# Optimization experiments

Measured on AMD Instinct MI355X. Metric: run time of the kernel, lower is better.

Reference implementation:

```python
import jax, jax.numpy as jnp
import numpy as np

TEMPERATURE = 0.1


def setup_inputs() -> dict:
    key = jax.random.key(0)
    k1, k2 = jax.random.split(key)
    N, T, D = 4096, 4, 256
    v_feat = jax.random.normal(k1, (N, D), dtype=jnp.float32)
    t_feat = jax.random.normal(k2, (N * T, D), dtype=jnp.float32)
    return {"v_feat": v_feat, "t_feat": t_feat}


def reference(v_feat, t_feat):
    N, D = v_feat.shape
    NT = t_feat.shape[0]
    T = NT // N

    # similarity matrix, scaled by temperature: [N, N*T]
    s_flat = (v_feat @ t_feat.T) / TEMPERATURE
    s = s_flat.reshape(N, N, T)

    # nominator: diagonal blocks s[i, i, :] -> logsumexp over T
    # (equivalent to (s * eye[:, :, None]).sum(dim=1))
    diag = jnp.diagonal(s, axis1=0, axis2=1).T  # [N, T]
    nominator = jax.nn.logsumexp(diag, axis=1)  # [N]

    # denominator: concat(s, s^T) along dim 1 -> [N, 2N, T] -> logsumexp over flat
    denom_in = jnp.concatenate([s, jnp.transpose(s, (1, 0, 2))], axis=1).reshape(N, -1)
    denominator = jax.nn.logsumexp(denom_in, axis=1)  # [N]

    mil_nce_loss = jnp.mean(denominator - nominator)

    # --- metrics (no grad), vectorized replacement of the python loop ---
    # rank[i, j] = index (into N*T columns) of the j-th largest score for row i
    rank = jnp.argsort(-s_flat, axis=1)  # [N, N*T], descending
    # column c belongs to video c // T; positive hit where that equals row index i
    hit = (rank // T) == jnp.arange(N)[:, None]  # [N, N*T] bool
    positions = jnp.arange(NT, dtype=jnp.float32)
    avg_rank = jnp.sum(hit.astype(jnp.float32) * positions, axis=1) / T
    recall1 = jnp.sum(hit[:, :1].astype(jnp.float32), axis=1) / T
    recall5 = jnp.sum(hit[:, :5].astype(jnp.float32), axis=1) / T
    recall10 = jnp.sum(hit[:, :10].astype(jnp.float32), axis=1) / T

    return (mil_nce_loss,
            jnp.mean(recall1), jnp.mean(recall5), jnp.mean(recall10),
            jnp.mean(avg_rank))
```

## Files before the change

### kernel.cpp

```cpp
#include <hip/hip_runtime.h>
#include <stdint.h>

#define N_V   4096
#define T_PER 4
#define NT    16384
#define D_K   256
#define SCALE 10.0f
#define LOG2E 1.44269504088896340736f
#define LN2   0.69314718055994530942f

#if defined(__has_builtin)
#if __has_builtin(__builtin_amdgcn_exp2f)
#define EXP2F(x) __builtin_amdgcn_exp2f(x)
#endif
#endif
#ifndef EXP2F
#define EXP2F(x) exp2f(x)
#endif

typedef __bf16 bf16x8 __attribute__((ext_vector_type(8)));
typedef float  f32x4  __attribute__((ext_vector_type(4)));

template<int C>
__device__ __forceinline__ float dppf(float v) {
  return __int_as_float(__builtin_amdgcn_update_dpp(
      0, __float_as_int(v), C, 0xf, 0xf, true));
}
template<int C>
__device__ __forceinline__ uint32_t dppu(uint32_t v) {
  return (uint32_t)__builtin_amdgcn_update_dpp(0, (int)v, C, 0xf, 0xf, true);
}
__device__ __forceinline__ float max16(float v) {
  v = fmaxf(v, dppf<0x121>(v));
  v = fmaxf(v, dppf<0x122>(v));
  v = fmaxf(v, dppf<0x124>(v));
  v = fmaxf(v, dppf<0x128>(v));
  return v;
}
__device__ __forceinline__ float sum16f(float v) {
  v += dppf<0x121>(v); v += dppf<0x122>(v);
  v += dppf<0x124>(v); v += dppf<0x128>(v);
  return v;
}
__device__ __forceinline__ uint32_t sum16u(uint32_t v) {
  v += dppu<0x121>(v); v += dppu<0x122>(v);
  v += dppu<0x124>(v); v += dppu<0x128>(v);
  return v;
}

__device__ __forceinline__ unsigned short f2bf(float f) {
  uint32_t u = __float_as_uint(f);
  u = (u + 0x7fffu + ((u >> 16) & 1u)) >> 16;
  return (unsigned short)u;
}

__global__ void k_prep(const float* __restrict__ v, const float* __restrict__ t,
                       unsigned short* __restrict__ Abf, unsigned short* __restrict__ Bbf,
                       float* __restrict__ thr, float* __restrict__ nom,
                       float* __restrict__ out) {
  const int tid = threadIdx.x, l = tid & 63, w = tid >> 6;
  const int i = blockIdx.x * 4 + w;
  if (blockIdx.x == 0 && tid < 5) out[tid] = 0.0f;
  const float AS = SCALE * LOG2E;

  float4 a = ((const float4*)(v + (size_t)i * D_K))[l];
  ushort4 oa;
  oa.x = f2bf(a.x * AS); oa.y = f2bf(a.y * AS);
  oa.z = f2bf(a.z * AS); oa.w = f2bf(a.w * AS);
  ((ushort4*)(Abf + (size_t)i * D_K))[l] = oa;

  float tv[T_PER];
#pragma unroll
  for (int tt = 0; tt < T_PER; ++tt) {
    float4 b = ((const float4*)(t + (size_t)(i * T_PER + tt) * D_K))[l];
    ushort4 ob;
    ob.x = f2bf(b.x); ob.y = f2bf(b.y); ob.z = f2bf(b.z); ob.w = f2bf(b.w);
    ((ushort4*)(Bbf + (size_t)(i * T_PER + tt) * D_K))[l] = ob;
    float d = a.x * b.x + a.y * b.y + a.z * b.z + a.w * b.w;
#pragma unroll
    for (int s = 1; s < 64; s <<= 1) d += __shfl_xor(d, s);
    tv[tt] = d * SCALE;
  }
  if (l == 0) {
    ((float4*)thr)[i] = make_float4(tv[0] * LOG2E, tv[1] * LOG2E,
                                    tv[2] * LOG2E, tv[3] * LOG2E);
    float m = fmaxf(fmaxf(tv[0], tv[1]), fmaxf(tv[2], tv[3]));
    float e = __expf(tv[0] - m) + __expf(tv[1] - m) + __expf(tv[2] - m) + __expf(tv[3] - m);
    nom[i] = m + __logf(e);
  }
}

__device__ __forceinline__ void gld16(const void* g, void* l) {
  __builtin_amdgcn_global_load_lds((const __attribute__((address_space(1))) void*)g,
                                   (__attribute__((address_space(3))) void*)l,
                                   16, 0, 0);
}

__global__ __launch_bounds__(256, 4) void k_gemm(
    const unsigned short* __restrict__ Abf, const unsigned short* __restrict__ Bbf,
    const float* __restrict__ thr,
    float* __restrict__ pmax, float* __restrict__ psum, uint4* __restrict__ pcnt,
    float* __restrict__ cmax, float* __restrict__ csum) {
  __shared__ __align__(16) unsigned short As[64 * 256];
  __shared__ float4   thrS[64];
  __shared__ float    rowMw[4][64], rowEw[4][64];
  __shared__ uint32_t rowCw[4][64];

  const int ct = blockIdx.x, rt = blockIdx.y;
  const int row0 = rt * 64, col0 = ct * 256;
  const int tid = threadIdx.x;
  const int l = tid & 63, w = tid >> 6;
  const int quad = l >> 4, nl = l & 15;

  if (tid < 64) thrS[tid] = ((const float4*)thr)[row0 + tid];

  const int lr = l >> 3, lc7 = l & 7;
  const int sc = lc7 ^ lr;
#pragma unroll
  for (int it = 0; it < 8; ++it) {
    int g = w * 8 + it;
    int rs = g >> 2, ks = g & 3;
    const unsigned short* ga =
        Abf + (size_t)(row0 + rs * 8 + lr) * D_K + ks * 64 + sc * 8;
    gld16(ga, (char*)As + g * 1024);
  }

  f32x4 acc[4][4];
#pragma unroll
  for (int i = 0; i < 4; ++i)
#pragma unroll
    for (int j = 0; j < 4; ++j) acc[i][j] = {0.f, 0.f, 0.f, 0.f};

  const unsigned short* pB[4];
#pragma unroll
  for (int j = 0; j < 4; ++j)
    pB[j] = Bbf + (size_t)(col0 + w * 64 + j * 16 + nl) * D_K + quad * 8;

  __syncthreads();

  bf16x8 bv[3][4];
#pragma unroll
  for (int j = 0; j < 4; ++j) bv[0][j] = *(const bf16x8*)(pB[j]);
#pragma unroll
  for (int j = 0; j < 4; ++j) bv[1][j] = *(const bf16x8*)(pB[j] + 32);

#pragma unroll
  for (int c = 0; c < 8; ++c) {
    if (c < 6) {
#pragma unroll
      for (int j = 0; j < 4; ++j)
        bv[(c + 2) % 3][j] = *(const bf16x8*)(pB[j] + (c + 2) * 32);
    }
    bf16x8 af[4];
#pragma unroll
    for (int i = 0; i < 4; ++i) {
      int r = i * 16 + nl;
      int rb = r & 7;
      int grp = (r >> 3) * 4 + (c >> 1);
      int cc = ((((c & 1) << 2) | quad) ^ rb);
      af[i] = *(const bf16x8*)((const char*)As + grp * 1024 + (rb * 8 + cc) * 16);
    }
#pragma unroll
    for (int i = 0; i < 4; ++i)
#pragma unroll
      for (int j = 0; j < 4; ++j)
        acc[i][j] = __builtin_amdgcn_mfma_f32_16x16x32_bf16(af[i], bv[c % 3][j],
                                                            acc[i][j], 0, 0, 0);
  }


#pragma unroll
  for (int i = 0; i < 4; ++i) {
#pragma unroll
    for (int r = 0; r < 4; ++r) {
      const int row = i * 16 + quad * 4 + r;
      float4 th = thrS[row];
      float s0 = acc[i][0][r], s1 = acc[i][1][r];
      float s2 = acc[i][2][r], s3 = acc[i][3][r];
      uint32_t c0 = (uint32_t)(s0 > th.x) + (uint32_t)(s1 > th.x)
                  + (uint32_t)(s2 > th.x) + (uint32_t)(s3 > th.x);
      uint32_t c1 = (uint32_t)(s0 > th.y) + (uint32_t)(s1 > th.y)
                  + (uint32_t)(s2 > th.y) + (uint32_t)(s3 > th.y);
      uint32_t c2 = (uint32_t)(s0 > th.z) + (uint32_t)(s1 > th.z)
                  + (uint32_t)(s2 > th.z) + (uint32_t)(s3 > th.z);
      uint32_t c3 = (uint32_t)(s0 > th.w) + (uint32_t)(s1 > th.w)
                  + (uint32_t)(s2 > th.w) + (uint32_t)(s3 > th.w);
      uint32_t c = c0 + (c1 << 8) + (c2 << 16) + (c3 << 24);
      c = sum16u(c);
      float m = fmaxf(fmaxf(s0, s1), fmaxf(s2, s3));
      m = max16(m);
      float e = (EXP2F(s0 - m) + EXP2F(s1 - m)) + (EXP2F(s2 - m) + EXP2F(s3 - m));
      e = sum16f(e);
      if (nl == 0) {
        rowMw[w][row] = m; rowEw[w][row] = e; rowCw[w][row] = c;
      }
    }
  }

#pragma unroll
  for (int j = 0; j < 4; ++j) {
    float m = -3.0e38f;
#pragma unroll
    for (int i = 0; i < 4; ++i)
#pragma unroll
      for (int r = 0; r < 4; ++r) m = fmaxf(m, acc[i][j][r]);
    m = fmaxf(m, __shfl_xor(m, 16));
    m = fmaxf(m, __shfl_xor(m, 32));
    float e = 0.f;
#pragma unroll
    for (int i = 0; i < 4; ++i)
#pragma unroll
      for (int r = 0; r < 4; ++r) e += EXP2F(acc[i][j][r] - m);
    e += __shfl_xor(e, 16);
    e += __shfl_xor(e, 32);
    if (quad == 0) {
      int colg = col0 + w * 64 + j * 16 + nl;
      size_t gi = (size_t)rt * NT + colg;
      cmax[gi] = m; csum[gi] = e;
    }
  }
  __syncthreads();

  if (tid < 64) {
    float M0 = rowMw[0][tid], M1 = rowMw[1][tid], M2 = rowMw[2][tid], M3 = rowMw[3][tid];
    float Mx = fmaxf(fmaxf(M0, M1), fmaxf(M2, M3));
    float Sx = rowEw[0][tid] * EXP2F(M0 - Mx) + rowEw[1][tid] * EXP2F(M1 - Mx)
             + rowEw[2][tid] * EXP2F(M2 - Mx) + rowEw[3][tid] * EXP2F(M3 - Mx);
    uint32_t c0 = 0, c1 = 0, c2 = 0, c3 = 0;
#pragma unroll
    for (int ww = 0; ww < 4; ++ww) {
      uint32_t cc = rowCw[ww][tid];
      c0 += cc & 0xffu; c1 += (cc >> 8) & 0xffu;
      c2 += (cc >> 16) & 0xffu; c3 += cc >> 24;
    }
    size_t gi = (size_t)ct * N_V + row0 + tid;
    pmax[gi] = Mx; psum[gi] = Sx; pcnt[gi] = make_uint4(c0, c1, c2, c3);
  }
}

__global__ void k_redfin(const float* __restrict__ pmax, const float* __restrict__ psum,
                         const uint4* __restrict__ pcnt,
                         const float* __restrict__ cmax, const float* __restrict__ csum,
                         const float* __restrict__ nom, float* __restrict__ out) {
  __shared__ float Lm[4][64], Ls[4][64];
  __shared__ uint4 Lc[4][64];
  __shared__ float CmH[2][256], CsH[2][256];
  __shared__ float rowM[64], rowS[64];
  __shared__ uint4 rowC[64];
  __shared__ float colM[256], colS[256];
  const int b = blockIdx.x, tid = threadIdx.x;
  const int l = tid & 63, w = tid >> 6;

  {
    int row = b * 64 + l;
    float mv[16];
#pragma unroll
    for (int k = 0; k < 16; ++k)
      mv[k] = pmax[(size_t)(w * 16 + k) * N_V + row];
    float tm[8];
#pragma unroll
    for (int k = 0; k < 8; ++k) tm[k] = fmaxf(mv[k], mv[k + 8]);
#pragma unroll
    for (int k = 0; k < 4; ++k) tm[k] = fmaxf(tm[k], tm[k + 4]);
    float M = fmaxf(fmaxf(tm[0], tm[1]), fmaxf(tm[2], tm[3]));
    float S = 0.f;
    uint32_t c0 = 0, c1 = 0, c2 = 0, c3 = 0;
#pragma unroll
    for (int k = 0; k < 16; ++k) {
      size_t idx = (size_t)(w * 16 + k) * N_V + row;
      S += psum[idx] * EXP2F(mv[k] - M);
      uint4 cc = pcnt[idx];
      c0 += cc.x; c1 += cc.y; c2 += cc.z; c3 += cc.w;
    }
    Lm[w][l] = M; Ls[w][l] = S; Lc[w][l] = make_uint4(c0, c1, c2, c3);
  }

  {
    int cc = tid & 127, h = tid >> 7;
#pragma unroll
    for (int half = 0; half < 2; ++half) {
      int colL = half * 128 + cc;
      int col = b * 256 + colL;
      float mv[32];
#pragma unroll
      for (int k = 0; k < 32; ++k)
        mv[k] = cmax[(size_t)(h * 32 + k) * NT + col];
      float tm[16];
#pragma unroll
      for (int k = 0; k < 16; ++k) tm[k] = fmaxf(mv[k], mv[k + 16]);
#pragma unroll
      for (int k = 0; k < 8; ++k) tm[k] = fmaxf(tm[k], tm[k + 8]);
#pragma unroll
      for (int k = 0; k < 4; ++k) tm[k] = fmaxf(tm[k], tm[k + 4]);
      float M = fmaxf(fmaxf(tm[0], tm[1]), fmaxf(tm[2], tm[3]));
      float S = 0.f;
#pragma unroll
      for (int k = 0; k < 32; ++k)
        S += csum[(size_t)(h * 32 + k) * NT + col] * EXP2F(mv[k] - M);
      CmH[h][colL] = M; CsH[h][colL] = S;
    }
  }
  __syncthreads();

  if (tid < 64) {
    float M0 = Lm[0][tid], M1 = Lm[1][tid], M2 = Lm[2][tid], M3 = Lm[3][tid];
    float Mx = fmaxf(fmaxf(M0, M1), fmaxf(M2, M3));
    float Sx = Ls[0][tid] * EXP2F(M0 - Mx) + Ls[1][tid] * EXP2F(M1 - Mx)
             + Ls[2][tid] * EXP2F(M2 - Mx) + Ls[3][tid] * EXP2F(M3 - Mx);
    uint4 C = Lc[0][tid];
#pragma unroll
    for (int ww = 1; ww < 4; ++ww) {
      uint4 cc = Lc[ww][tid];
      C.x += cc.x; C.y += cc.y; C.z += cc.z; C.w += cc.w;
    }
    rowM[tid] = Mx; rowS[tid] = Sx; rowC[tid] = C;
  }
  {
    float M0 = CmH[0][tid], S0 = CsH[0][tid];
    float M1 = CmH[1][tid], S1 = CsH[1][tid];
    float Mx = fmaxf(M0, M1);
    float Sx = S0 * EXP2F(M0 - Mx) + S1 * EXP2F(M1 - Mx);
    colM[tid] = Mx; colS[tid] = Sx;
  }
  __syncthreads();

  if (tid < 64) {
    int row = b * 64 + tid;
    float M = rowM[tid], S = rowS[tid];
    float cm0 = colM[tid * 4 + 0], cm1 = colM[tid * 4 + 1];
    float cm2 = colM[tid * 4 + 2], cm3 = colM[tid * 4 + 3];
    float cs0 = colS[tid * 4 + 0], cs1 = colS[tid * 4 + 1];
    float cs2 = colS[tid * 4 + 2], cs3 = colS[tid * 4 + 3];
    float Mp = fmaxf(M, fmaxf(fmaxf(cm0, cm1), fmaxf(cm2, cm3)));
    float tot = S * EXP2F(M - Mp)
              + cs0 * EXP2F(cm0 - Mp) + cs1 * EXP2F(cm1 - Mp)
              + cs2 * EXP2F(cm2 - Mp) + cs3 * EXP2F(cm3 - Mp);
    float ll = LN2 * (Mp + __log2f(tot)) - nom[row];
    uint4 c = rowC[tid];
    float ar  = (float)(c.x + c.y + c.z + c.w) * 0.25f;
    float r1  = (float)((c.x < 1u) + (c.y < 1u) + (c.z < 1u) + (c.w < 1u)) * 0.25f;
    float r5  = (float)((c.x < 5u) + (c.y < 5u) + (c.z < 5u) + (c.w < 5u)) * 0.25f;
    float r10 = (float)((c.x < 10u) + (c.y < 10u) + (c.z < 10u) + (c.w < 10u)) * 0.25f;
    float vals[5] = {ll, r1, r5, r10, ar};
#pragma unroll
    for (int k = 0; k < 5; ++k) {
      float v = vals[k];
#pragma unroll
      for (int d = 1; d < 64; d <<= 1) v += __shfl_xor(v, d);
      if (tid == 0) atomicAdd(&out[k], v * (1.0f / N_V));
    }
  }
}

extern "C" void kernel_launch(void* const* d_in, const int* in_sizes, int n_in,
                              void* d_out, int out_size, void* d_ws, size_t ws_size,
                              hipStream_t stream) {
  const float* v = (const float*)d_in[0];
  const float* t = (const float*)d_in[1];
  char* p = (char*)d_ws;
  unsigned short* Abf = (unsigned short*)p; p += (size_t)N_V * D_K * 2;
  unsigned short* Bbf = (unsigned short*)p; p += (size_t)NT * D_K * 2;
  float* thr  = (float*)p;    p += (size_t)N_V * 4 * 4;
  float* nom  = (float*)p;    p += (size_t)N_V * 4;
  float* pmax = (float*)p;    p += (size_t)64 * N_V * 4;
  float* psum = (float*)p;    p += (size_t)64 * N_V * 4;
  uint4* pcnt = (uint4*)p;    p += (size_t)64 * N_V * 16;
  float* cmaxp = (float*)p;   p += (size_t)64 * NT * 4;
  float* csump = (float*)p;   p += (size_t)64 * NT * 4;

  k_prep<<<N_V / 4, 256, 0, stream>>>(v, t, Abf, Bbf, thr, nom, (float*)d_out);
  dim3 g(NT / 256, N_V / 64);
  k_gemm<<<g, 256, 0, stream>>>(Abf, Bbf, thr, pmax, psum, pcnt, cmaxp, csump);
  k_redfin<<<64, 256, 0, stream>>>(pmax, psum, pcnt, cmaxp, csump, nom, (float*)d_out);
}
```

Measured before the change: 156.5 us.

## Reuse A tile across two column tiles per block and widen reduction grid

Each GEMM block now processes two 256-column tiles while loading the 64-row A tile into LDS only once. This halves the block count and the redundant A loads, and it raises wave priority around the MFMA loop. The final reduction kernel is re-partitioned from 64 blocks to 256 blocks with less serial work per thread, aiming to fill more CUs. In exchange, the GEMM grid has fewer blocks, which may lower occupancy and load balance, and there is an extra barrier per tile.

Result: slower. 187.2 us (+19.6%).

```diff
diff --git a/kernel.cpp b/kernel.cpp
--- a/kernel.cpp
+++ b/kernel.cpp
@@ -107,7 +107,7 @@
   __shared__ uint32_t rowCw[4][64];
 
   const int ct = blockIdx.x, rt = blockIdx.y;
-  const int row0 = rt * 64, col0 = ct * 256;
+  const int row0 = rt * 64;
   const int tid = threadIdx.x;
   const int l = tid & 63, w = tid >> 6;
   const int quad = l >> 4, nl = l & 15;
@@ -125,116 +125,124 @@
     gld16(ga, (char*)As + g * 1024);
   }
 
-  f32x4 acc[4][4];
-#pragma unroll
-  for (int i = 0; i < 4; ++i)
-#pragma unroll
-    for (int j = 0; j < 4; ++j) acc[i][j] = {0.f, 0.f, 0.f, 0.f};
-
-  const unsigned short* pB[4];
-#pragma unroll
-  for (int j = 0; j < 4; ++j)
-    pB[j] = Bbf + (size_t)(col0 + w * 64 + j * 16 + nl) * D_K + quad * 8;
-
-  __syncthreads();
-
-  bf16x8 bv[3][4];
-#pragma unroll
-  for (int j = 0; j < 4; ++j) bv[0][j] = *(const bf16x8*)(pB[j]);
-#pragma unroll
-  for (int j = 0; j < 4; ++j) bv[1][j] = *(const bf16x8*)(pB[j] + 32);
-
-#pragma unroll
-  for (int c = 0; c < 8; ++c) {
-    if (c < 6) {
-#pragma unroll
-      for (int j = 0; j < 4; ++j)
-        bv[(c + 2) % 3][j] = *(const bf16x8*)(pB[j] + (c + 2) * 32);
-    }
-    bf16x8 af[4];
+#pragma unroll
+  for (int tile = 0; tile < 2; ++tile) {
+    const int col0 = ct * 512 + tile * 256;
+    const int ctp = ct * 2 + tile;
+
+    f32x4 acc[4][4];
+#pragma unroll
+    for (int i = 0; i < 4; ++i)
+#pragma unroll
+      for (int j = 0; j < 4; ++j) acc[i][j] = {0.f, 0.f, 0.f, 0.f};
+
+    const unsigned short* pB[4];
+#pragma unroll
+    for (int j = 0; j < 4; ++j)
+      pB[j] = Bbf + (size_t)(col0 + w * 64 + j * 16 + nl) * D_K + quad * 8;
+
+    bf16x8 bv[3][4];
+#pragma unroll
+    for (int j = 0; j < 4; ++j) bv[0][j] = *(const bf16x8*)(pB[j]);
+#pragma unroll
+    for (int j = 0; j < 4; ++j) bv[1][j] = *(const bf16x8*)(pB[j] + 32);
+
+    __syncthreads();
+
+    __builtin_amdgcn_s_setprio(1);
+#pragma unroll
+    for (int c = 0; c < 8; ++c) {
+      if (c < 6) {
+#pragma unroll
+        for (int j = 0; j < 4; ++j)
+          bv[(c + 2) % 3][j] = *(const bf16x8*)(pB[j] + (c + 2) * 32);
+      }
+      bf16x8 af[4];
+#pragma unroll
+      for (int i = 0; i < 4; ++i) {
+        int r = i * 16 + nl;
+        int rb = r & 7;
+        int grp = (r >> 3) * 4 + (c >> 1);
+        int cc = ((((c & 1) << 2) | quad) ^ rb);
+        af[i] = *(const bf16x8*)((const char*)As + grp * 1024 + (rb * 8 + cc) * 16);
+      }
+#pragma unroll
+      for (int i = 0; i < 4; ++i)
+#pragma unroll
+        for (int j = 0; j < 4; ++j)
+          acc[i][j] = __builtin_amdgcn_mfma_f32_16x16x32_bf16(af[i], bv[c % 3][j],
+                                                              acc[i][j], 0, 0, 0);
+    }
+    __builtin_amdgcn_s_setprio(0);
+
+
 #pragma unroll
     for (int i = 0; i < 4; ++i) {
-      int r = i * 16 + nl;
-      int rb = r & 7;
-      int grp = (r >> 3) * 4 + (c >> 1);
-      int cc = ((((c & 1) << 2) | quad) ^ rb);
-      af[i] = *(const bf16x8*)((const char*)As + grp * 1024 + (rb * 8 + cc) * 16);
-    }
-#pragma unroll
-    for (int i = 0; i < 4; ++i)
-#pragma unroll
-      for (int j = 0; j < 4; ++j)
-        acc[i][j] = __builtin_amdgcn_mfma_f32_16x16x32_bf16(af[i], bv[c % 3][j],
-                                                            acc[i][j], 0, 0, 0);
-  }
-
-
-#pragma unroll
-  for (int i = 0; i < 4; ++i) {
-#pragma unroll
-    for (int r = 0; r < 4; ++r) {
-      const int row = i * 16 + quad * 4 + r;
-      float4 th = thrS[row];
-      float s0 = acc[i][0][r], s1 = acc[i][1][r];
-      float s2 = acc[i][2][r], s3 = acc[i][3][r];
-      uint32_t c0 = (uint32_t)(s0 > th.x) + (uint32_t)(s1 > th.x)
-                  + (uint32_t)(s2 > th.x) + (uint32_t)(s3 > th.x);
-      uint32_t c1 = (uint32_t)(s0 > th.y) + (uint32_t)(s1 > th.y)
-                  + (uint32_t)(s2 > th.y) + (uint32_t)(s3 > th.y);
-      uint32_t c2 = (uint32_t)(s0 > th.z) + (uint32_t)(s1 > th.z)
-                  + (uint32_t)(s2 > th.z) + (uint32_t)(s3 > th.z);
-      uint32_t c3 = (uint32_t)(s0 > th.w) + (uint32_t)(s1 > th.w)
-                  + (uint32_t)(s2 > th.w) + (uint32_t)(s3 > th.w);
-      uint32_t c = c0 + (c1 << 8) + (c2 << 16) + (c3 << 24);
-      c = sum16u(c);
-      float m = fmaxf(fmaxf(s0, s1), fmaxf(s2, s3));
-      m = max16(m);
-      float e = (EXP2F(s0 - m) + EXP2F(s1 - m)) + (EXP2F(s2 - m) + EXP2F(s3 - m));
-      e = sum16f(e);
-      if (nl == 0) {
-        rowMw[w][row] = m; rowEw[w][row] = e; rowCw[w][row] = c;
-      }
-    }
-  }
-
-#pragma unroll
-  for (int j = 0; j < 4; ++j) {
-    float m = -3.0e38f;
-#pragma unroll
-    for (int i = 0; i < 4; ++i)
-#pragma unroll
-      for (int r = 0; r < 4; ++r) m = fmaxf(m, acc[i][j][r]);
-    m = fmaxf(m, __shfl_xor(m, 16));
-    m = fmaxf(m, __shfl_xor(m, 32));
-    float e = 0.f;
-#pragma unroll
-    for (int i = 0; i < 4; ++i)
-#pragma unroll
-      for (int r = 0; r < 4; ++r) e += EXP2F(acc[i][j][r] - m);
-    e += __shfl_xor(e, 16);
-    e += __shfl_xor(e, 32);
-    if (quad == 0) {
-      int colg = col0 + w * 64 + j * 16 + nl;
-      size_t gi = (size_t)rt * NT + colg;
-      cmax[gi] = m; csum[gi] = e;
-    }
-  }
-  __syncthreads();
-
-  if (tid < 64) {
-    float M0 = rowMw[0][tid], M1 = rowMw[1][tid], M2 = rowMw[2][tid], M3 = rowMw[3][tid];
-    float Mx = fmaxf(fmaxf(M0, M1), fmaxf(M2, M3));
-    float Sx = rowEw[0][tid] * EXP2F(M0 - Mx) + rowEw[1][tid] * EXP2F(M1 - Mx)
-             + rowEw[2][tid] * EXP2F(M2 - Mx) + rowEw[3][tid] * EXP2F(M3 - Mx);
-    uint32_t c0 = 0, c1 = 0, c2 = 0, c3 = 0;
-#pragma unroll
-    for (int ww = 0; ww < 4; ++ww) {
-      uint32_t cc = rowCw[ww][tid];
-      c0 += cc & 0xffu; c1 += (cc >> 8) & 0xffu;
-      c2 += (cc >> 16) & 0xffu; c3 += cc >> 24;
-    }
-    size_t gi = (size_t)ct * N_V + row0 + tid;
-    pmax[gi] = Mx; psum[gi] = Sx; pcnt[gi] = make_uint4(c0, c1, c2, c3);
+#pragma unroll
+      for (int r = 0; r < 4; ++r) {
+        const int row = i * 16 + quad * 4 + r;
+        float4 th = thrS[row];
+        float s0 = acc[i][0][r], s1 = acc[i][1][r];
+        float s2 = acc[i][2][r], s3 = acc[i][3][r];
+        uint32_t c0 = (uint32_t)(s0 > th.x) + (uint32_t)(s1 > th.x)
+                    + (uint32_t)(s2 > th.x) + (uint32_t)(s3 > th.x);
+        uint32_t c1 = (uint32_t)(s0 > th.y) + (uint32_t)(s1 > th.y)
+                    + (uint32_t)(s2 > th.y) + (uint32_t)(s3 > th.y);
+        uint32_t c2 = (uint32_t)(s0 > th.z) + (uint32_t)(s1 > th.z)
+                    + (uint32_t)(s2 > th.z) + (uint32_t)(s3 > th.z);
+        uint32_t c3 = (uint32_t)(s0 > th.w) + (uint32_t)(s1 > th.w)
+                    + (uint32_t)(s2 > th.w) + (uint32_t)(s3 > th.w);
+        uint32_t c = c0 + (c1 << 8) + (c2 << 16) + (c3 << 24);
+        c = sum16u(c);
+        float m = fmaxf(fmaxf(s0, s1), fmaxf(s2, s3));
+        m = max16(m);
+        float e = (EXP2F(s0 - m) + EXP2F(s1 - m)) + (EXP2F(s2 - m) + EXP2F(s3 - m));
+        e = sum16f(e);
+        if (nl == 0) {
+          rowMw[w][row] = m; rowEw[w][row] = e; rowCw[w][row] = c;
+        }
+      }
+    }
+
+#pragma unroll
+    for (int j = 0; j < 4; ++j) {
+      float m = -3.0e38f;
+#pragma unroll
+      for (int i = 0; i < 4; ++i)
+#pragma unroll
+        for (int r = 0; r < 4; ++r) m = fmaxf(m, acc[i][j][r]);
+      m = fmaxf(m, __shfl_xor(m, 16));
+      m = fmaxf(m, __shfl_xor(m, 32));
+      float e = 0.f;
+#pragma unroll
+      for (int i = 0; i < 4; ++i)
+#pragma unroll
+        for (int r = 0; r < 4; ++r) e += EXP2F(acc[i][j][r] - m);
+      e += __shfl_xor(e, 16);
+      e += __shfl_xor(e, 32);
+      if (quad == 0) {
+        int colg = col0 + w * 64 + j * 16 + nl;
+        size_t gi = (size_t)rt * NT + colg;
+        cmax[gi] = m; csum[gi] = e;
+      }
+    }
+    __syncthreads();
+
+    if (tid < 64) {
+      float M0 = rowMw[0][tid], M1 = rowMw[1][tid], M2 = rowMw[2][tid], M3 = rowMw[3][tid];
+      float Mx = fmaxf(fmaxf(M0, M1), fmaxf(M2, M3));
+      float Sx = rowEw[0][tid] * EXP2F(M0 - Mx) + rowEw[1][tid] * EXP2F(M1 - Mx)
+               + rowEw[2][tid] * EXP2F(M2 - Mx) + rowEw[3][tid] * EXP2F(M3 - Mx);
+      uint32_t c0 = 0, c1 = 0, c2 = 0, c3 = 0;
+#pragma unroll
+      for (int ww = 0; ww < 4; ++ww) {
+        uint32_t cc = rowCw[ww][tid];
+        c0 += cc & 0xffu; c1 += (cc >> 8) & 0xffu;
+        c2 += (cc >> 16) & 0xffu; c3 += cc >> 24;
+      }
+      size_t gi = (size_t)ctp * N_V + row0 + tid;
+      pmax[gi] = Mx; psum[gi] = Sx; pcnt[gi] = make_uint4(c0, c1, c2, c3);
+    }
   }
 }
 
@@ -242,21 +250,40 @@
                          const uint4* __restrict__ pcnt,
                          const float* __restrict__ cmax, const float* __restrict__ csum,
                          const float* __restrict__ nom, float* __restrict__ out) {
-  __shared__ float Lm[4][64], Ls[4][64];
-  __shared__ uint4 Lc[4][64];
-  __shared__ float CmH[2][256], CsH[2][256];
-  __shared__ float rowM[64], rowS[64];
-  __shared__ uint4 rowC[64];
-  __shared__ float colM[256], colS[256];
+  __shared__ float Lm[16][16], Ls[16][16];
+  __shared__ uint4 Lc[16][16];
+  __shared__ float Cm[4][64], Cs[4][64];
+  __shared__ float colM[64], colS[64];
   const int b = blockIdx.x, tid = threadIdx.x;
-  const int l = tid & 63, w = tid >> 6;
 
   {
-    int row = b * 64 + l;
+    const int rloc = tid & 15, chunk = tid >> 4;
+    const int row = b * 16 + rloc;
+    float mv[4];
+#pragma unroll
+    for (int k = 0; k < 4; ++k)
+      mv[k] = pmax[(size_t)(chunk * 4 + k) * N_V + row];
+    float M = fmaxf(fmaxf(mv[0], mv[1]), fmaxf(mv[2], mv[3]));
+    float S = 0.f;
+    uint32_t c0 = 0, c1 = 0, c2 = 0, c3 = 0;
+#pragma unroll
+    for (int k = 0; k < 4; ++k) {
+      size_t idx = (size_t)(chunk * 4 + k) * N_V + row;
+      S += psum[idx] * EXP2F(mv[k] - M);
+      uint4 cc = pcnt[idx];
+      c0 += cc.x; c1 += cc.y; c2 += cc.z; c3 += cc.w;
+    }
+    Lm[chunk][rloc] = M; Ls[chunk][rloc] = S;
+    Lc[chunk][rloc] = make_uint4(c0, c1, c2, c3);
+  }
+
+  {
+    const int cloc = tid & 63, h = tid >> 6;
+    const int col = b * 64 + cloc;
     float mv[16];
 #pragma unroll
     for (int k = 0; k < 16; ++k)
-      mv[k] = pmax[(size_t)(w * 16 + k) * N_V + row];
+      mv[k] = cmax[(size_t)(h * 16 + k) * NT + col];
     float tm[8];
 #pragma unroll
     for (int k = 0; k < 8; ++k) tm[k] = fmaxf(mv[k], mv[k + 8]);
@@ -264,89 +291,57 @@
     for (int k = 0; k < 4; ++k) tm[k] = fmaxf(tm[k], tm[k + 4]);
     float M = fmaxf(fmaxf(tm[0], tm[1]), fmaxf(tm[2], tm[3]));
     float S = 0.f;
-    uint32_t c0 = 0, c1 = 0, c2 = 0, c3 = 0;
-#pragma unroll
-    for (int k = 0; k < 16; ++k) {
-      size_t idx = (size_t)(w * 16 + k) * N_V + row;
-      S += psum[idx] * EXP2F(mv[k] - M);
-      uint4 cc = pcnt[idx];
-      c0 += cc.x; c1 += cc.y; c2 += cc.z; c3 += cc.w;
-    }
-    Lm[w][l] = M; Ls[w][l] = S; Lc[w][l] = make_uint4(c0, c1, c2, c3);
-  }
-
-  {
-    int cc = tid & 127, h = tid >> 7;
-#pragma unroll
-    for (int half = 0; half < 2; ++half) {
-      int colL = half * 128 + cc;
-      int col = b * 256 + colL;
-      float mv[32];
-#pragma unroll
-      for (int k = 0; k < 32; ++k)
-        mv[k] = cmax[(size_t)(h * 32 + k) * NT + col];
-      float tm[16];
-#pragma unroll
-      for (int k = 0; k < 16; ++k) tm[k] = fmaxf(mv[k], mv[k + 16]);
-#pragma unroll
-      for (int k = 0; k < 8; ++k) tm[k] = fmaxf(tm[k], tm[k + 8]);
-#pragma unroll
-      for (int k = 0; k < 4; ++k) tm[k] = fmaxf(tm[k], tm[k + 4]);
-      float M = fmaxf(fmaxf(tm[0], tm[1]), fmaxf(tm[2], tm[3]));
-      float S = 0.f;
-#pragma unroll
-      for (int k = 0; k < 32; ++k)
-        S += csum[(size_t)(h * 32 + k) * NT + col] * EXP2F(mv[k] - M);
-      CmH[h][colL] = M; CsH[h][colL] = S;
-    }
+#pragma unroll
+    for (int k = 0; k < 16; ++k)
+      S += csum[(size_t)(h * 16 + k) * NT + col] * EXP2F(mv[k] - M);
+    Cm[h][cloc] = M; Cs[h][cloc] = S;
   }
   __syncthreads();
 
   if (tid < 64) {
-    float M0 = Lm[0][tid], M1 = Lm[1][tid], M2 = Lm[2][tid], M3 = Lm[3][tid];
+    float M0 = Cm[0][tid], M1 = Cm[1][tid], M2 = Cm[2][tid], M3 = Cm[3][tid];
     float Mx = fmaxf(fmaxf(M0, M1), fmaxf(M2, M3));
-    float Sx = Ls[0][tid] * EXP2F(M0 - Mx) + Ls[1][tid] * EXP2F(M1 - Mx)
-             + Ls[2][tid] * EXP2F(M2 - Mx) + Ls[3][tid] * EXP2F(M3 - Mx);
-    uint4 C = Lc[0][tid];
-#pragma unroll
-    for (int ww = 1; ww < 4; ++ww) {
-      uint4 cc = Lc[ww][tid];
-      C.x += cc.x; C.y += cc.y; C.z += cc.z; C.w += cc.w;
-    }
-    rowM[tid] = Mx; rowS[tid] = Sx; rowC[tid] = C;
-  }
-  {
-    float M0 = CmH[0][tid], S0 = CsH[0][tid];
-    float M1 = CmH[1][tid], S1 = CsH[1][tid];
-    float Mx = fmaxf(M0, M1);
-    float Sx = S0 * EXP2F(M0 - Mx) + S1 * EXP2F(M1 - Mx);
+    float Sx = Cs[0][tid] * EXP2F(M0 - Mx) + Cs[1][tid] * EXP2F(M1 - Mx)
+             + Cs[2][tid] * EXP2F(M2 - Mx) + Cs[3][tid] * EXP2F(M3 - Mx);
     colM[tid] = Mx; colS[tid] = Sx;
   }
+  float rM = -3.0e38f, rS = 0.f;
+  uint4 rC = make_uint4(0, 0, 0, 0);
+  if (tid < 16) {
+    float m8[8];
+#pragma unroll
+    for (int c = 0; c < 8; ++c) m8[c] = fmaxf(Lm[c][tid], Lm[c + 8][tid]);
+#pragma unroll
+    for (int c = 0; c < 4; ++c) m8[c] = fmaxf(m8[c], m8[c + 4]);
+    rM = fmaxf(fmaxf(m8[0], m8[1]), fmaxf(m8[2], m8[3]));
+#pragma unroll
+    for (int c = 0; c < 16; ++c) {
+      rS += Ls[c][tid] * EXP2F(Lm[c][tid] - rM);
+      uint4 cc = Lc[c][tid];
+      rC.x += cc.x; rC.y += cc.y; rC.z += cc.z; rC.w += cc.w;
+    }
+  }
   __syncthreads();
 
-  if (tid < 64) {
-    int row = b * 64 + tid;
-    float M = rowM[tid], S = rowS[tid];
+  if (tid < 16) {
+    int row = b * 16 + tid;
     float cm0 = colM[tid * 4 + 0], cm1 = colM[tid * 4 + 1];
     float cm2 = colM[tid * 4 + 2], cm3 = colM[tid * 4 + 3];
     float cs0 = colS[tid * 4 + 0], cs1 = colS[tid * 4 + 1];
     float cs2 = colS[tid * 4 + 2], cs3 = colS[tid * 4 + 3];
-    float Mp = fmaxf(M, fmaxf(fmaxf(cm0, cm1), fmaxf(cm2, cm3)));
-    float tot = S * EXP2F(M - Mp)
+    float Mp = fmaxf(rM, fmaxf(fmaxf(cm0, cm1), fmaxf(cm2, cm3)));
+    float tot = rS * EXP2F(rM - Mp)
               + cs0 * EXP2F(cm0 - Mp) + cs1 * EXP2F(cm1 - Mp)
               + cs2 * EXP2F(cm2 - Mp) + cs3 * EXP2F(cm3 - Mp);
     float ll = LN2 * (Mp + __log2f(tot)) - nom[row];
-    uint4 c = rowC[tid];
-    float ar  = (float)(c.x + c.y + c.z + c.w) * 0.25f;
-    float r1  = (float)((c.x < 1u) + (c.y < 1u) + (c.z < 1u) + (c.w < 1u)) * 0.25f;
-    float r5  = (float)((c.x < 5u) + (c.y < 5u) + (c.z < 5u) + (c.w < 5u)) * 0.25f;
-    float r10 = (float)((c.x < 10u) + (c.y < 10u) + (c.z < 10u) + (c.w < 10u)) * 0.25f;
+    float ar  = (float)(rC.x + rC.y + rC.z + rC.w) * 0.25f;
+    float r1  = (float)((rC.x < 1u) + (rC.y < 1u) + (rC.z < 1u) + (rC.w < 1u)) * 0.25f;
+    float r5  = (float)((rC.x < 5u) + (rC.y < 5u) + (rC.z < 5u) + (rC.w < 5u)) * 0.25f;
+    float r10 = (float)((rC.x < 10u) + (rC.y < 10u) + (rC.z < 10u) + (rC.w < 10u)) * 0.25f;
     float vals[5] = {ll, r1, r5, r10, ar};
 #pragma unroll
     for (int k = 0; k < 5; ++k) {
-      float v = vals[k];
-#pragma unroll
-      for (int d = 1; d < 64; d <<= 1) v += __shfl_xor(v, d);
+      float v = sum16f(vals[k]);
       if (tid == 0) atomicAdd(&out[k], v * (1.0f / N_V));
     }
   }
@@ -369,7 +364,8 @@
   float* csump = (float*)p;   p += (size_t)64 * NT * 4;
 
   k_prep<<<N_V / 4, 256, 0, stream>>>(v, t, Abf, Bbf, thr, nom, (float*)d_out);
-  dim3 g(NT / 256, N_V / 64);
+  dim3 g(NT / 512, N_V / 64);
   k_gemm<<<g, 256, 0, stream>>>(Abf, Bbf, thr, pmax, psum, pcnt, cmaxp, csump);
-  k_redfin<<<64, 256, 0, stream>>>(pmax, psum, pcnt, cmaxp, csump, nom, (float*)d_out);
-}
+  k_redfin<<<N_V / 16, 256, 0, stream>>>(pmax, psum, pcnt, cmaxp, csump, nom,
+                                         (float*)d_out);
+}
```
